# Optimization experiments

Measured on AMD Instinct MI355X. Metric: run time of the kernel, lower is better.

## Reference

```python
import jax, jax.numpy as jnp
import numpy as np

WINDOW_SIZE = 11
SIGMA = 1.5
K2 = 0.03
PAD = WINDOW_SIZE // 2


def _gaussian_window(size, sigma):
    coords = np.arange(size, dtype=np.float32) - size // 2
    g = np.exp(-coords ** 2 / (2.0 * sigma ** 2))
    g = g / g.sum()
    w2d = np.outer(g, g)  # [size, size]
    return jnp.asarray(w2d[None, None], dtype=jnp.float32)  # [1,1,size,size]


def _blur(x, w):
    # x: [B,1,H,W], w: [1,1,k,k]; SAME zero padding, matches F.conv2d(padding=k//2)
    return jax.lax.conv_general_dilated(
        x, w, window_strides=(1, 1), padding=[(PAD, PAD), (PAD, PAD)],
        dimension_numbers=("NCHW", "OIHW", "NCHW"))


def setup_inputs() -> dict:
    key = jax.random.key(0)
    k1, k2 = jax.random.split(key)
    B, C, H, W = 32, 1, 512, 512
    inp = jax.random.uniform(k1, (B, C, H, W), dtype=jnp.float32)
    tgt = jax.random.uniform(k2, (B, C, H, W), dtype=jnp.float32)
    mask = jnp.ones((B, C, H, W), dtype=jnp.float32)
    window = _gaussian_window(WINDOW_SIZE, SIGMA)
    return {"input": inp, "target": tgt, "mask": mask, "window": window}


def reference(input, target, mask, window):
    # mask application (mask path is always exercised, matching the torch code)
    inp = input * mask
    tgt = target * mask

    mw = _blur(mask, window) + 1e-08  # blurred mask normalizer

    mu_i = _blur(inp, window) / mw
    mu_t = _blur(tgt, window) / mw

    sigma_i_sq = _blur(inp * inp, window) / mw - mu_i * mu_i
    sigma_t_sq = _blur(tgt * tgt, window) / mw - mu_t * mu_t
    sigma_it = _blur(inp * tgt, window) / mw - mu_i * mu_t

    L = jnp.maximum(jnp.max(inp), jnp.max(tgt))
    C2 = (K2 * L) ** 2
    C3 = C2 / 2.0

    sigma_i = jnp.sqrt(jax.nn.relu(sigma_i_sq) + 1e-12)
    sigma_t = jnp.sqrt(jax.nn.relu(sigma_t_sq) + 1e-12)

    structure_map = (sigma_it + C3) / (sigma_i * sigma_t + C3 + 1e-08)
    return 1.0 - jnp.mean(structure_map)
```

## Files before the change

kernel.cpp:

```cpp
#include <hip/hip_runtime.h>
#include <math.h>

#define H 512
#define W 512
#define NPIX (32LL*512*512)

#define VSTR 42
#define VCH(wid,ch,u,c) uni[(wid)*2016 + (ch)*336 + (u)*VSTR + (c)]

__device__ inline unsigned encf(float f) {
    unsigned u = __float_as_uint(f);
    return (u & 0x80000000u) ? ~u : (u | 0x80000000u);
}
__device__ inline float decf(unsigned e) {
    unsigned u = (e & 0x80000000u) ? (e ^ 0x80000000u) : ~e;
    return __uint_as_float(u);
}

__global__ __launch_bounds__(256) void maxred_kernel(
        const float* __restrict__ in, const float* __restrict__ tg,
        const float* __restrict__ mk, unsigned* __restrict__ mx) {
    const float4* in4 = (const float4*)in;
    const float4* tg4 = (const float4*)tg;
    const float4* mk4 = (const float4*)mk;
    long long n4 = NPIX / 4;
    long long idx = (long long)blockIdx.x * blockDim.x + threadIdx.x;
    long long stride = (long long)gridDim.x * blockDim.x;
    float ma = -INFINITY, mb = -INFINITY;
    for (long long i = idx; i < n4; i += stride) {
        float4 a = in4[i], b = tg4[i], c = mk4[i];
        ma = fmaxf(ma, fmaxf(fmaxf(a.x * c.x, a.y * c.y), fmaxf(a.z * c.z, a.w * c.w)));
        mb = fmaxf(mb, fmaxf(fmaxf(b.x * c.x, b.y * c.y), fmaxf(b.z * c.z, b.w * c.w)));
    }
    float m = fmaxf(ma, mb);
    #pragma unroll
    for (int off = 32; off; off >>= 1) m = fmaxf(m, __shfl_down(m, off, 64));
    __shared__ float smax[4];
    int lane = threadIdx.x & 63, wid = threadIdx.x >> 6;
    if (lane == 0) smax[wid] = m;
    __syncthreads();
    if (threadIdx.x == 0) {
        float r = fmaxf(fmaxf(smax[0], smax[1]), fmaxf(smax[2], smax[3]));
        atomicMax(mx, encf(r));
    }
}

__global__ __launch_bounds__(256, 4) void ssim_kernel(
        const float* __restrict__ in, const float* __restrict__ tg,
        const float* __restrict__ mk, const float* __restrict__ win,
        const unsigned* __restrict__ mxp, double* __restrict__ sum) {
    __shared__ __align__(16) float uni[8064];
    __shared__ float ssum[4];

    int t = threadIdx.x;
    int lane = t & 63, wid = t >> 6;

    float rs = 0.f;
    if (lane < 11) {
        #pragma unroll
        for (int j = 0; j < 11; j++) rs += win[lane * 11 + j];
    }
    float wk[11];
    #pragma unroll
    for (int k = 0; k < 11; k++)
        wk[k] = __uint_as_float(__builtin_amdgcn_readfirstlane(
                    __float_as_uint(__shfl(rs, k, 64))));

    float L = decf(*mxp);
    float C3 = 0.5f * (0.03f * L) * (0.03f * L);

    int img = blockIdx.z;
    int y0w = blockIdx.y * 32 + wid * 8;
    int x0  = blockIdx.x * 32;
    const size_t base = (size_t)img * H * W;
    const float* __restrict__ inb = in + base;
    const float* __restrict__ tgb = tg + base;
    const float* __restrict__ mkb = mk + base;

    if (lane < 42) {
        int x = x0 - 5 + lane;
        bool inx = (unsigned)x < (unsigned)W;
        int xc = inx ? x : 0;
        float xs = inx ? 1.f : 0.f;
        int ybase = y0w - 5;

        float acc[6][8];
        #pragma unroll
        for (int ch = 0; ch < 6; ch++)
            #pragma unroll
            for (int u = 0; u < 8; u++) acc[ch][u] = 0.f;

        if (ybase >= 0 && ybase <= H - 18) {
            size_t g = (size_t)ybase * W + xc;
            #pragma unroll
            for (int j = 0; j < 18; j++) {
                float iv = inb[g], tv = tgb[g], m = mkb[g] * xs;
                g += W;
                float a = iv * m, b = tv * m;
                float v[6] = { m, a, b, a * a, b * b, a * b };
                #pragma unroll
                for (int u = 0; u < 8; u++) {
                    int k = j - u;
                    if (k >= 0 && k < 11) {
                        float w = wk[k];
                        #pragma unroll
                        for (int ch = 0; ch < 6; ch++)
                            acc[ch][u] = fmaf(w, v[ch], acc[ch][u]);
                    }
                }
            }
        } else {
            #pragma unroll
            for (int j = 0; j < 18; j++) {
                int y = ybase + j;
                bool yok = (unsigned)y < (unsigned)H;
                size_t g = (size_t)(yok ? y : 0) * W + xc;
                float sc = yok ? xs : 0.f;
                float iv = inb[g], tv = tgb[g], m = mkb[g] * sc;
                float a = iv * m, b = tv * m;
                float v[6] = { m, a, b, a * a, b * b, a * b };
                #pragma unroll
                for (int u = 0; u < 8; u++) {
                    int k = j - u;
                    if (k >= 0 && k < 11) {
                        float w = wk[k];
                        #pragma unroll
                        for (int ch = 0; ch < 6; ch++)
                            acc[ch][u] = fmaf(w, v[ch], acc[ch][u]);
                    }
                }
            }
        }
        #pragma unroll
        for (int u = 0; u < 8; u++)
            #pragma unroll
            for (int ch = 0; ch < 6; ch++) VCH(wid, ch, u, lane) = acc[ch][u];
    }

    __builtin_amdgcn_wave_barrier();
    asm volatile("s_waitcnt lgkmcnt(0)" ::: "memory");
    __builtin_amdgcn_sched_barrier(0);

    int r = lane >> 3, c0 = (lane & 7) << 2;
    float hs[6][4];
    #pragma unroll
    for (int ch = 0; ch < 6; ch++) {
        float Wl[14];
        #pragma unroll
        for (int q = 0; q < 7; q++) {
            float2 v = *(const float2*)&VCH(wid, ch, r, c0 + 2 * q);
            Wl[2 * q] = v.x; Wl[2 * q + 1] = v.y;
        }
        #pragma unroll
        for (int u = 0; u < 4; u++) {
            float h = 0.f;
            #pragma unroll
            for (int k = 0; k < 11; k++) h = fmaf(wk[k], Wl[u + k], h);
            hs[ch][u] = h;
        }
    }

    float lsum = 0.f;
    #pragma unroll
    for (int u = 0; u < 4; u++) {
        float h1 = hs[1][u], h2 = hs[2][u];
        float mw = hs[0][u] + 1e-8f;
        float mw2 = mw * mw;
        float e12 = 1e-12f * mw2;
        float Xi = fmaxf(fmaf(hs[3][u], mw, -h1 * h1), 0.f) + e12;
        float Xt = fmaxf(fmaf(hs[4][u], mw, -h2 * h2), 0.f) + e12;
        float num = fmaf(hs[5][u], mw, -h1 * h2) + C3 * mw2;
        float den = __builtin_amdgcn_sqrtf(Xi * Xt) + (C3 + 1e-8f) * mw2;
        lsum += num * __builtin_amdgcn_rcpf(den);
    }

    #pragma unroll
    for (int off = 32; off; off >>= 1) lsum += __shfl_down(lsum, off, 64);
    if (lane == 0) ssum[wid] = lsum;
    __syncthreads();
    if (t == 0) {
        float tot = ssum[0] + ssum[1] + ssum[2] + ssum[3];
        atomicAdd(sum, (double)tot);
    }
}

__global__ void fin_kernel(const double* __restrict__ sum, float* __restrict__ out) {
    out[0] = 1.0f - (float)(*sum / (double)NPIX);
}

extern "C" void kernel_launch(void* const* d_in, const int* in_sizes, int n_in,
                              void* d_out, int out_size, void* d_ws, size_t ws_size,
                              hipStream_t stream) {
    const float* in  = (const float*)d_in[0];
    const float* tg  = (const float*)d_in[1];
    const float* mk  = (const float*)d_in[2];
    const float* win = (const float*)d_in[3];
    float* out = (float*)d_out;

    double*   dsum = (double*)d_ws;
    unsigned* dmax = (unsigned*)((char*)d_ws + 8);

    hipMemsetAsync(d_ws, 0, 12, stream);
    maxred_kernel<<<2048, 256, 0, stream>>>(in, tg, mk, dmax);
    ssim_kernel<<<dim3(16, 16, 32), 256, 0, stream>>>(in, tg, mk, win, dmax, dsum);
    fin_kernel<<<1, 1, 0, stream>>>(dsum, out);
}
```

Before: 159.9 us.

## Raise SSIM occupancy, prefetch rows, widen max reduction, double reduction grid

Several separate tweaks are bundled here. The SSIM kernel's launch bound goes from 4 to 5 blocks per CU, and the separable window weights are now built through shared memory with a block barrier instead of cross-lane shuffles. The interior vertical pass prefetches input rows four ahead in a rotating register buffer to hide load latency. The max-reduction kernel keeps per-component float4 maxima to shorten the dependency chain and launches twice as many blocks. The extra prefetch registers together with the tighter occupancy target may cause register spills.

```diff
diff --git a/kernel.cpp b/kernel.cpp
--- a/kernel.cpp
+++ b/kernel.cpp
@@ -5,8 +5,7 @@
 #define W 512
 #define NPIX (32LL*512*512)
 
-#define VSTR 42
-#define VCH(wid,ch,u,c) uni[(wid)*2016 + (ch)*336 + (u)*VSTR + (c)]
+#define VCH(wid,ch,u,c) uni[(wid)*2016 + (ch)*336 + (u)*42 + (c)]
 
 __device__ inline unsigned encf(float f) {
     unsigned u = __float_as_uint(f);
@@ -26,13 +25,17 @@
     long long n4 = NPIX / 4;
     long long idx = (long long)blockIdx.x * blockDim.x + threadIdx.x;
     long long stride = (long long)gridDim.x * blockDim.x;
-    float ma = -INFINITY, mb = -INFINITY;
+    float4 A = make_float4(-INFINITY, -INFINITY, -INFINITY, -INFINITY);
+    float4 B = A;
     for (long long i = idx; i < n4; i += stride) {
         float4 a = in4[i], b = tg4[i], c = mk4[i];
-        ma = fmaxf(ma, fmaxf(fmaxf(a.x * c.x, a.y * c.y), fmaxf(a.z * c.z, a.w * c.w)));
-        mb = fmaxf(mb, fmaxf(fmaxf(b.x * c.x, b.y * c.y), fmaxf(b.z * c.z, b.w * c.w)));
-    }
-    float m = fmaxf(ma, mb);
+        A.x = fmaxf(A.x, a.x * c.x); A.y = fmaxf(A.y, a.y * c.y);
+        A.z = fmaxf(A.z, a.z * c.z); A.w = fmaxf(A.w, a.w * c.w);
+        B.x = fmaxf(B.x, b.x * c.x); B.y = fmaxf(B.y, b.y * c.y);
+        B.z = fmaxf(B.z, b.z * c.z); B.w = fmaxf(B.w, b.w * c.w);
+    }
+    float m = fmaxf(fmaxf(fmaxf(A.x, A.y), fmaxf(A.z, A.w)),
+                    fmaxf(fmaxf(B.x, B.y), fmaxf(B.z, B.w)));
     #pragma unroll
     for (int off = 32; off; off >>= 1) m = fmaxf(m, __shfl_down(m, off, 64));
     __shared__ float smax[4];
@@ -45,29 +48,31 @@
     }
 }
 
-__global__ __launch_bounds__(256, 4) void ssim_kernel(
+__global__ __launch_bounds__(256, 5) void ssim_kernel(
         const float* __restrict__ in, const float* __restrict__ tg,
         const float* __restrict__ mk, const float* __restrict__ win,
         const unsigned* __restrict__ mxp, double* __restrict__ sum) {
     __shared__ __align__(16) float uni[8064];
+    __shared__ float gw[11];
     __shared__ float ssum[4];
 
     int t = threadIdx.x;
     int lane = t & 63, wid = t >> 6;
 
-    float rs = 0.f;
-    if (lane < 11) {
-        #pragma unroll
-        for (int j = 0; j < 11; j++) rs += win[lane * 11 + j];
-    }
-    float wk[11];
-    #pragma unroll
-    for (int k = 0; k < 11; k++)
-        wk[k] = __uint_as_float(__builtin_amdgcn_readfirstlane(
-                    __float_as_uint(__shfl(rs, k, 64))));
-
+    if (t < 11) {
+        float s = 0.f;
+        #pragma unroll
+        for (int j = 0; j < 11; j++) s += win[t * 11 + j];
+        gw[t] = s;
+    }
     float L = decf(*mxp);
     float C3 = 0.5f * (0.03f * L) * (0.03f * L);
+    __syncthreads();
+
+    float wk[11];
+    #pragma unroll
+    for (int k = 0; k < 11; k++)
+        wk[k] = __uint_as_float(__builtin_amdgcn_readfirstlane(__float_as_uint(gw[k])));
 
     int img = blockIdx.z;
     int y0w = blockIdx.y * 32 + wid * 8;
@@ -92,10 +97,19 @@
 
         if (ybase >= 0 && ybase <= H - 18) {
             size_t g = (size_t)ybase * W + xc;
+            float pi[4], pt[4], pm[4];
+            #pragma unroll
+            for (int p = 0; p < 4; p++) {
+                pi[p] = inb[g]; pt[p] = tgb[g]; pm[p] = mkb[g];
+                g += W;
+            }
             #pragma unroll
             for (int j = 0; j < 18; j++) {
-                float iv = inb[g], tv = tgb[g], m = mkb[g] * xs;
-                g += W;
+                float iv = pi[j & 3], tv = pt[j & 3], m = pm[j & 3] * xs;
+                if (j + 4 < 18) {
+                    pi[j & 3] = inb[g]; pt[j & 3] = tgb[g]; pm[j & 3] = mkb[g];
+                    g += W;
+                }
                 float a = iv * m, b = tv * m;
                 float v[6] = { m, a, b, a * a, b * b, a * b };
                 #pragma unroll
@@ -201,7 +215,7 @@
     unsigned* dmax = (unsigned*)((char*)d_ws + 8);
 
     hipMemsetAsync(d_ws, 0, 12, stream);
-    maxred_kernel<<<2048, 256, 0, stream>>>(in, tg, mk, dmax);
+    maxred_kernel<<<4096, 256, 0, stream>>>(in, tg, mk, dmax);
     ssim_kernel<<<dim3(16, 16, 32), 256, 0, stream>>>(in, tg, mk, win, dmax, dsum);
     fin_kernel<<<1, 1, 0, stream>>>(dsum, out);
 }
```

After: 187.0 us. 1.17x slower.
